# Kernel tuning notes

Hardware: AMD Instinct MI355X
Metric: run time of the kernel (lower is better)

The kernel has to match this reference:

```python
import jax, jax.numpy as jnp
import numpy as np

C = 256
H = W = 64
B = 8


def setup_inputs() -> dict:
    key = jax.random.key(0)
    ks = jax.random.split(key, 9)
    s = 1.0 / np.sqrt(C)
    x = jax.random.normal(ks[0], (B, C, H, W), dtype=jnp.float32)
    Wq = jax.random.normal(ks[1], (C, C), dtype=jnp.float32) * s
    bq = jnp.zeros((C,), dtype=jnp.float32)
    Wk = jax.random.normal(ks[2], (C, C), dtype=jnp.float32) * s
    bk = jnp.zeros((C,), dtype=jnp.float32)
    Wv = jax.random.normal(ks[3], (C, C), dtype=jnp.float32) * s
    bv = jnp.zeros((C,), dtype=jnp.float32)
    Wp = jax.random.normal(ks[4], (C, C), dtype=jnp.float32) * s
    bp = jnp.zeros((C,), dtype=jnp.float32)
    return {"x": x, "Wq": Wq, "bq": bq, "Wk": Wk, "bk": bk,
            "Wv": Wv, "bv": bv, "Wp": Wp, "bp": bp}


def reference(x, Wq, bq, Wk, bk, Wv, bv, Wp, bp):
    # NOTE: the original forward never calls self.norm, so GroupNorm is omitted.
    Bv_, Cv, Hv, Wv_ = x.shape
    N = Hv * Wv_
    xf = x.reshape(Bv_, Cv, N)  # [B, C, N]
    # 1x1 convs == per-pixel linear over channels
    q = jnp.einsum('oc,bcn->bno', Wq, xf) + bq            # [B, N, C]
    k = jnp.einsum('oc,bcn->bon', Wk, xf) + bk[:, None]   # [B, C, N]
    v = jnp.einsum('oc,bcn->bno', Wv, xf) + bv            # [B, N, C]
    scale = Cv ** (-0.5)
    attn = jnp.einsum('bnc,bcm->bnm', q, k) * scale       # [B, N, N]
    attn = jax.nn.softmax(attn, axis=-1)
    h = jnp.einsum('bnm,bmc->bnc', attn, v)               # [B, N, C]
    h = h.transpose(0, 2, 1).reshape(Bv_, Cv, Hv, Wv_)
    proj = jnp.einsum('oc,bcn->bon', Wp, xf) + bp[:, None]
    proj = proj.reshape(Bv_, Cv, Hv, Wv_)
    # residual uses proj(x) (applied to the INPUT), as in the original code
    return h + proj
```

## Files before the change

### kernel.cpp

```cpp
#include <hip/hip_runtime.h>

typedef __attribute__((ext_vector_type(8))) short short8;
typedef __attribute__((ext_vector_type(4))) short short4v;
typedef __attribute__((ext_vector_type(4))) float floatx4;
typedef unsigned int u32;

#define CC 256
#define NN 4096
#define NB 8

static __device__ __forceinline__ float b2f(ushort u) {
    union { unsigned int i; float f; } c;
    c.i = ((unsigned int)u) << 16;
    return c.f;
}

static __device__ __forceinline__ ushort f2bf(float f) {
    union { float f; unsigned int u; } c;
    c.f = f;
    unsigned int u = c.u;
    u += 0x7fffu + ((u >> 16) & 1u);
    return (ushort)(u >> 16);
}

static __device__ __forceinline__ short8 load8(const void* p, size_t idx, bool isbf) {
    if (isbf) {
        return *(const short8*)((const ushort*)p + idx);
    } else {
        const float* f = (const float*)p + idx;
        floatx4 a = *(const floatx4*)f;
        floatx4 b = *(const floatx4*)(f + 4);
        short8 r;
        #pragma unroll
        for (int j = 0; j < 4; j++) {
            ((ushort*)&r)[j]     = f2bf(a[j]);
            ((ushort*)&r)[j + 4] = f2bf(b[j]);
        }
        return r;
    }
}

static __device__ __forceinline__ float loadS(const void* p, size_t idx, bool isbf) {
    return isbf ? b2f(((const ushort*)p)[idx]) : ((const float*)p)[idx];
}

static __device__ __forceinline__ bool detect_bf16(const void* x) {
    const ushort* xu = (const ushort*)x;
    int cnt = 0;
    #pragma unroll
    for (int j = 0; j < 8; j++) {
        ushort u = xu[(size_t)j * 1048576];
        int e = (u >> 7) & 0xFF;
        cnt += ((e >= 100 && e <= 141) || (u & 0x7FFF) == 0) ? 1 : 0;
    }
    return cnt >= 7;
}

static __device__ __forceinline__ void gll16(const ushort* g, ushort* l) {
    __builtin_amdgcn_global_load_lds(
        (const __attribute__((address_space(1))) u32*)g,
        (__attribute__((address_space(3))) u32*)l, 16, 0, 0);
}

__global__ __launch_bounds__(256) void projkvpq(
    const void* __restrict__ x,
    const void* __restrict__ Wk, const void* __restrict__ bk,
    const void* __restrict__ Wv, const void* __restrict__ bv,
    const void* __restrict__ Wp, const void* __restrict__ bp,
    const void* __restrict__ Wq, const void* __restrict__ bq,
    ushort* __restrict__ k_ws, ushort* __restrict__ v_ws,
    ushort* __restrict__ q_ws, float* __restrict__ out, int b0)
{
    __shared__ __align__(16) ushort A_lds[4][64 * 40];
    __shared__ __align__(16) ushort Bt_lds[64 * 40];
    __shared__ __align__(16) ushort T_lds[64 * 72];

    const bool isbf = detect_bf16(x);
    const int tid  = threadIdx.x;
    const int wave = tid >> 6;
    const int lane = tid & 63;
    const int l16  = lane & 15;
    const int quad = lane >> 4;

    const int n0 = blockIdx.x * 64;
    const int o0 = blockIdx.y * 64;
    const int bl = blockIdx.z;
    const int b  = b0 + bl;

    floatx4 zero4 = {0.f, 0.f, 0.f, 0.f};
    floatx4 acc[4][4];
    #pragma unroll
    for (int w = 0; w < 4; w++)
        #pragma unroll
        for (int t = 0; t < 4; t++) acc[w][t] = zero4;

    const void* Ws[4] = {Wk, Wv, Wp, Wq};

    for (int k0 = 0; k0 < CC; k0 += 32) {
        __syncthreads();
        {
            int row = tid >> 2, c8 = (tid & 3) * 8;
            #pragma unroll
            for (int w = 0; w < 4; w++)
                *(short8*)&A_lds[w][row * 40 + c8] =
                    load8(Ws[w], (size_t)(o0 + row) * CC + k0 + c8, isbf);
        }
        {
            int c = tid >> 3, n8 = (tid & 7) * 8;
            short8 xv = load8(x, ((size_t)b * CC + k0 + c) * NN + n0 + n8, isbf);
            #pragma unroll
            for (int j = 0; j < 8; j++)
                Bt_lds[(n8 + j) * 40 + c] = ((ushort*)&xv)[j];
        }
        __syncthreads();

        short8 af[4];
        #pragma unroll
        for (int w = 0; w < 4; w++)
            af[w] = *(const short8*)&A_lds[w][(wave * 16 + l16) * 40 + quad * 8];
        #pragma unroll
        for (int t = 0; t < 4; t++) {
            short8 bf = *(const short8*)&Bt_lds[(t * 16 + l16) * 40 + quad * 8];
            #pragma unroll
            for (int w = 0; w < 4; w++)
                acc[w][t] = __builtin_amdgcn_mfma_f32_16x16x32_bf16(af[w], bf, acc[w][t], 0, 0, 0);
        }
    }

    float biasv[4][4];
    const void* Bs[4] = {bk, bv, bp, bq};
    #pragma unroll
    for (int w = 0; w < 4; w++)
        #pragma unroll
        for (int r = 0; r < 4; r++)
            biasv[w][r] = loadS(Bs[w], (size_t)(o0 + wave * 16 + quad * 4 + r), isbf);

    __syncthreads();
    #pragma unroll
    for (int t = 0; t < 4; t++)
        #pragma unroll
        for (int r = 0; r < 4; r++)
            T_lds[(t * 16 + l16) * 72 + wave * 16 + quad * 4 + r] =
                f2bf(acc[0][t][r] + biasv[0][r]);
    __syncthreads();
    for (int u = tid; u < 512; u += 256) {
        int n = u >> 3, o8 = (u & 7) * 8;
        *(short8*)&k_ws[((size_t)bl * NN + n0 + n) * CC + o0 + o8] =
            *(const short8*)&T_lds[n * 72 + o8];
    }

    __syncthreads();
    #pragma unroll
    for (int t = 0; t < 4; t++)
        #pragma unroll
        for (int r = 0; r < 4; r++)
            T_lds[(t * 16 + l16) * 72 + wave * 16 + quad * 4 + r] =
                f2bf((acc[3][t][r] + biasv[3][r]) * 0.0625f);
    __syncthreads();
    for (int u = tid; u < 512; u += 256) {
        int n = u >> 3, o8 = (u & 7) * 8;
        *(short8*)&q_ws[((size_t)bl * NN + n0 + n) * CC + o0 + o8] =
            *(const short8*)&T_lds[n * 72 + o8];
    }

    __syncthreads();
    #pragma unroll
    for (int t = 0; t < 4; t++)
        #pragma unroll
        for (int r = 0; r < 4; r++)
            T_lds[(wave * 16 + quad * 4 + r) * 72 + t * 16 + l16] =
                f2bf(acc[1][t][r] + biasv[1][r]);
    __syncthreads();
    for (int u = tid; u < 512; u += 256) {
        int o = u >> 3, n8 = (u & 7) * 8;
        *(short8*)&v_ws[((size_t)bl * CC + o0 + o) * NN + n0 + n8] =
            *(const short8*)&T_lds[o * 72 + n8];
    }

    #pragma unroll
    for (int t = 0; t < 4; t++)
        #pragma unroll
        for (int r = 0; r < 4; r++)
            out[((size_t)b * CC + o0 + wave * 16 + quad * 4 + r) * NN +
                n0 + t * 16 + l16] = acc[2][t][r] + biasv[2][r];
}

__global__ __launch_bounds__(512) void attn_mfma(
    const ushort* __restrict__ q_ws, const ushort* __restrict__ k_ws,
    const ushort* __restrict__ v_ws, float* __restrict__ out,
    float* __restrict__ po, float* __restrict__ ml, int b0, int nsplit)
{
    __shared__ __align__(16) ushort lds[33792];
    ushort* K_lds  = lds;
    ushort* Vt_lds = lds + 8192;
    ushort* P_lds  = lds + 16384;
    float*  Tf     = (float*)lds;

    const int tid  = threadIdx.x;
    const int wave = tid >> 6;
    const int lane = tid & 63;
    const int l16  = lane & 15;
    const int quad = lane >> 4;
    const int bl = blockIdx.y;
    const int b  = b0 + bl;
    const int n0 = blockIdx.x * 256;
    const int hs = blockIdx.z;

    floatx4 zero4 = {0.f, 0.f, 0.f, 0.f};

    const ushort* qp = q_ws + ((size_t)bl * NN + n0 + wave * 32 + l16) * CC;
    short8 qf[2][8];
    #pragma unroll
    for (int f = 0; f < 2; f++)
        #pragma unroll
        for (int s = 0; s < 8; s++)
            qf[f][s] = *(const short8*)&qp[(size_t)(f * 16) * CC + s * 32 + quad * 8];

    const ushort* kp = k_ws + (size_t)bl * NN * CC;
    const ushort* vp = v_ws + (size_t)bl * CC * NN;

    floatx4 Oacc[2][16];
    #pragma unroll
    for (int f = 0; f < 2; f++)
        #pragma unroll
        for (int t = 0; t < 16; t++) Oacc[f][t] = zero4;
    float mrow[2] = {-1e30f, -1e30f}, lrow[2] = {0.f, 0.f};

    const int NT  = (NN / 32) / nsplit;
    const int it0 = hs * NT;

    #pragma unroll 1
    for (int it = it0; it < it0 + NT; ++it) {
        const int m0 = it * 32;
        __syncthreads();

        #pragma unroll
        for (int i = 0; i < 2; i++) {
            int c = wave * 2 + i;
            {
                int row = c * 2 + (lane >> 5);
                int sw  = (lane & 31) ^ (row & 7);
                gll16(kp + (size_t)(m0 + row) * CC + sw * 8, K_lds + c * 512);
            }
            {
                int ch = c * 16 + (lane >> 2);
                gll16(vp + (size_t)ch * NN + m0 + (lane & 3) * 8, Vt_lds + c * 512);
            }
        }
        __syncthreads();

        floatx4 S[2][2];
        S[0][0] = zero4; S[0][1] = zero4; S[1][0] = zero4; S[1][1] = zero4;
        #pragma unroll
        for (int t = 0; t < 2; t++) {
            int row = t * 16 + l16;
            int rsw = row & 7;
            #pragma unroll
            for (int s = 0; s < 8; s++) {
                short8 kf = *(const short8*)&K_lds[row * 256 + ((s * 4 + quad) ^ rsw) * 8];
                S[0][t] = __builtin_amdgcn_mfma_f32_16x16x32_bf16(kf, qf[0][s], S[0][t], 0, 0, 0);
                S[1][t] = __builtin_amdgcn_mfma_f32_16x16x32_bf16(kf, qf[1][s], S[1][t], 0, 0, 0);
            }
        }

        float mx[2];
        #pragma unroll
        for (int f = 0; f < 2; f++) {
            float m = fmaxf(fmaxf(fmaxf(S[f][0][0], S[f][0][1]),
                                  fmaxf(S[f][0][2], S[f][0][3])),
                            fmaxf(fmaxf(S[f][1][0], S[f][1][1]),
                                  fmaxf(S[f][1][2], S[f][1][3])));
            m = fmaxf(m, __shfl_xor(m, 16, 64));
            m = fmaxf(m, __shfl_xor(m, 32, 64));
            mx[f] = m;
        }

        if (__any((mx[0] - mrow[0] > 8.0f) || (mx[1] - mrow[1] > 8.0f))) {
            float a[2][4];
            #pragma unroll
            for (int f = 0; f < 2; f++) {
                float mn = fmaxf(mrow[f], mx[f]);
                float al = __expf(mrow[f] - mn);
                mrow[f] = mn;
                lrow[f] *= al;
                #pragma unroll
                for (int r = 0; r < 4; r++) a[f][r] = __shfl(al, quad * 4 + r, 64);
            }
            #pragma unroll
            for (int f = 0; f < 2; f++)
                #pragma unroll
                for (int ct = 0; ct < 16; ct++)
                    #pragma unroll
                    for (int r = 0; r < 4; r++)
                        Oacc[f][ct][r] *= a[f][r];
        }

        #pragma unroll
        for (int f = 0; f < 2; f++) {
            short4v w0, w1;
            float rs = 0.f;
            #pragma unroll
            for (int r = 0; r < 4; r++) {
                float p0 = __expf(S[f][0][r] - mrow[f]);
                float p1 = __expf(S[f][1][r] - mrow[f]);
                rs += p0 + p1;
                ((ushort*)&w0)[r] = f2bf(p0);
                ((ushort*)&w1)[r] = f2bf(p1);
            }
            rs += __shfl_xor(rs, 16, 64);
            rs += __shfl_xor(rs, 32, 64);
            lrow[f] += rs;
            int base = wave * 1280 + (f * 16 + l16) * 40 + quad * 4;
            *(short4v*)&P_lds[base]      = w0;
            *(short4v*)&P_lds[base + 16] = w1;
        }

        asm volatile("s_waitcnt lgkmcnt(0)" ::: "memory");
        __builtin_amdgcn_sched_barrier(0);

        short8 pf0 = *(const short8*)&P_lds[wave * 1280 + l16 * 40 + quad * 8];
        short8 pf1 = *(const short8*)&P_lds[wave * 1280 + (16 + l16) * 40 + quad * 8];
        #pragma unroll
        for (int ct = 0; ct < 16; ct++) {
            int ch = ct * 16 + l16;
            short8 vf = *(const short8*)&Vt_lds[ch * 32 + quad * 8];
            Oacc[0][ct] = __builtin_amdgcn_mfma_f32_16x16x32_bf16(pf0, vf, Oacc[0][ct], 0, 0, 0);
            Oacc[1][ct] = __builtin_amdgcn_mfma_f32_16x16x32_bf16(pf1, vf, Oacc[1][ct], 0, 0, 0);
        }
    }

    if (nsplit == 1) {
        float linv[2][4];
        #pragma unroll
        for (int f = 0; f < 2; f++) {
            float li = 1.0f / lrow[f];
            #pragma unroll
            for (int r = 0; r < 4; r++) linv[f][r] = __shfl(li, quad * 4 + r, 64);
        }
        #pragma unroll
        for (int c0 = 0; c0 < 4; c0++) {
            __syncthreads();
            #pragma unroll
            for (int j = 0; j < 4; j++) {
                int ct = c0 * 4 + j;
                #pragma unroll
                for (int f = 0; f < 2; f++)
                    #pragma unroll
                    for (int r = 0; r < 4; r++)
                        Tf[(j * 16 + l16) * 264 + wave * 32 + f * 16 + quad * 4 + r] =
                            Oacc[f][ct][r] * linv[f][r];
            }
            __syncthreads();
            #pragma unroll
            for (int i = 0; i < 8; i++) {
                int u = tid + i * 512;
                int chl = u >> 6, col4 = (u & 63) * 4;
                size_t gi = ((size_t)b * CC + c0 * 64 + chl) * NN + n0 + col4;
                floatx4 pv = *(const floatx4*)&out[gi];
                floatx4 tv = *(const floatx4*)&Tf[chl * 264 + col4];
                pv[0] += tv[0]; pv[1] += tv[1]; pv[2] += tv[2]; pv[3] += tv[3];
                *(floatx4*)&out[gi] = pv;
            }
        }
    } else {
        const int pidx = (hs * NB + b) * (NN / 256) + blockIdx.x;
        float* pO = po + (size_t)pidx * (256 * 256);
        if (quad == 0) {
            #pragma unroll
            for (int f = 0; f < 2; f++) {
                int row = wave * 32 + f * 16 + l16;
                ml[(size_t)pidx * 512 + row]       = mrow[f];
                ml[(size_t)pidx * 512 + 256 + row] = lrow[f];
            }
        }
        #pragma unroll
        for (int c0 = 0; c0 < 4; c0++) {
            __syncthreads();
            #pragma unroll
            for (int j = 0; j < 4; j++) {
                int ct = c0 * 4 + j;
                #pragma unroll
                for (int f = 0; f < 2; f++)
                    #pragma unroll
                    for (int r = 0; r < 4; r++)
                        Tf[(j * 16 + l16) * 264 + wave * 32 + f * 16 + quad * 4 + r] =
                            Oacc[f][ct][r];
            }
            __syncthreads();
            #pragma unroll
            for (int i = 0; i < 8; i++) {
                int u = tid + i * 512;
                int chl = u >> 6, col4 = (u & 63) * 4;
                *(floatx4*)&pO[(size_t)(c0 * 64 + chl) * 256 + col4] =
                    *(const floatx4*)&Tf[chl * 264 + col4];
            }
        }
    }
}

__global__ __launch_bounds__(256) void attn_merge(
    const float* __restrict__ po, const float* __restrict__ ml,
    float* __restrict__ out, int b0)
{
    __shared__ float sm[4][256];
    const int ntile = blockIdx.x;
    const int b = b0 + blockIdx.y;
    const int NT2 = NN / 256;
    const int p0 = (0 * NB + b) * NT2 + ntile;
    const int p1 = (1 * NB + b) * NT2 + ntile;
    const float* O0 = po + (size_t)p0 * (256 * 256);
    const float* O1 = po + (size_t)p1 * (256 * 256);
    const int tid = threadIdx.x;
    sm[0][tid] = ml[(size_t)p0 * 512 + tid];
    sm[1][tid] = ml[(size_t)p0 * 512 + 256 + tid];
    sm[2][tid] = ml[(size_t)p1 * 512 + tid];
    sm[3][tid] = ml[(size_t)p1 * 512 + 256 + tid];
    __syncthreads();

    const int c = tid;
    float* op = out + ((size_t)b * CC + c) * NN + ntile * 256;
    const float* a = O0 + (size_t)c * 256;
    const float* d = O1 + (size_t)c * 256;
    #pragma unroll 4
    for (int r4 = 0; r4 < 256; r4 += 4) {
        floatx4 va = *(const floatx4*)&a[r4];
        floatx4 vd = *(const floatx4*)&d[r4];
        floatx4 vo = *(const floatx4*)&op[r4];
        #pragma unroll
        for (int j = 0; j < 4; j++) {
            int row = r4 + j;
            float m0 = sm[0][row], l0 = sm[1][row];
            float m1 = sm[2][row], l1 = sm[3][row];
            float M  = fmaxf(m0, m1);
            float w0 = __expf(m0 - M), w1 = __expf(m1 - M);
            float L  = l0 * w0 + l1 * w1;
            vo[j] += (va[j] * w0 + vd[j] * w1) / L;
        }
        *(floatx4*)&op[r4] = vo;
    }
}

extern "C" void kernel_launch(void* const* d_in, const int* in_sizes, int n_in,
                              void* d_out, int out_size, void* d_ws, size_t ws_size,
                              hipStream_t stream) {
    int xi = 0;
    for (int i = 0; i < n_in; i++)
        if (in_sizes[i] == NB * CC * NN) xi = i;

    const void *x, *Wq, *bq, *Wk, *bk, *Wv, *bv, *Wp, *bp;
    if (xi == 0) {
        x  = d_in[0];
        Wq = d_in[1]; bq = d_in[2];
        Wk = d_in[3]; bk = d_in[4];
        Wv = d_in[5]; bv = d_in[6];
        Wp = d_in[7]; bp = d_in[8];
    } else {
        int wi[4], bi[4], nw = 0, nb = 0;
        for (int i = 0; i < n_in; i++) {
            if (i == xi) continue;
            if (in_sizes[i] == CC * CC) { if (nw < 4) wi[nw++] = i; }
            else                        { if (nb < 4) bi[nb++] = i; }
        }
        x  = d_in[xi];
        Wk = d_in[wi[0]]; Wp = d_in[wi[1]]; Wq = d_in[wi[2]]; Wv = d_in[wi[3]];
        bk = d_in[bi[0]]; bp = d_in[bi[1]]; bq = d_in[bi[2]]; bv = d_in[bi[3]];
    }

    float*  out = (float*)d_out;
    ushort* ws  = (ushort*)d_ws;

    const size_t tsz_b = (size_t)NN * CC;
    int BC = 8;
    while (BC > 1 && (size_t)BC * tsz_b * 2 * 3 > ws_size) BC >>= 1;
    ushort* k_ws = ws;
    ushort* v_ws = ws + (size_t)BC * tsz_b;
    ushort* q_ws = ws + 2 * (size_t)BC * tsz_b;

    const size_t base_bytes = (size_t)3 * BC * tsz_b * 2;
    const size_t po_elems   = (size_t)2 * NB * (NN / 256) * 256 * 256;
    const size_t ml_elems   = (size_t)2 * NB * (NN / 256) * 512;
    const int nsplit = (BC == 8 &&
                        ws_size >= base_bytes + (po_elems + ml_elems) * 4) ? 2 : 1;
    float* po = (float*)(ws + 3 * (size_t)BC * tsz_b);
    float* ml = po + po_elems;

    for (int c0 = 0; c0 < NB; c0 += BC) {
        projkvpq<<<dim3(NN / 64, CC / 64, BC), dim3(256), 0, stream>>>(
            x, Wk, bk, Wv, bv, Wp, bp, Wq, bq, k_ws, v_ws, q_ws, out, c0);
        attn_mfma<<<dim3(NN / 256, BC, nsplit), dim3(512), 0, stream>>>(
            q_ws, k_ws, v_ws, out, po, ml, c0, nsplit);
        if (nsplit == 2)
            attn_merge<<<dim3(NN / 256, BC), dim3(256), 0, stream>>>(
                po, ml, out, c0);
    }
}
```

Baseline: 380.6 us.

## Double-buffer K/V tiles in attention loop to overlap loads with MFMA

Splits the K and V shared-memory tiles into two buffers and prefetches the next key block while computing on the current one. A partial vmcnt wait keeps only the current tile's loads outstanding, and raw barriers replace the two __syncthreads per iteration. This hides global-to-LDS latency behind the QK and PV MFMA work. In exchange, LDS use grows from about 66KB to 84KB, which may reduce blocks per CU, and correctness depends on the hand-counted vmcnt value.

```diff
diff --git a/kernel.cpp b/kernel.cpp
--- a/kernel.cpp
+++ b/kernel.cpp
@@ -190,10 +190,12 @@
     const ushort* __restrict__ v_ws, float* __restrict__ out,
     float* __restrict__ po, float* __restrict__ ml, int b0, int nsplit)
 {
-    __shared__ __align__(16) ushort lds[33792];
-    ushort* K_lds  = lds;
-    ushort* Vt_lds = lds + 8192;
-    ushort* P_lds  = lds + 16384;
+    __shared__ __align__(16) ushort lds[43008];
+    ushort* K0_lds = lds;
+    ushort* K1_lds = lds + 8192;
+    ushort* V0_lds = lds + 16384;
+    ushort* V1_lds = lds + 24576;
+    ushort* P_lds  = lds + 32768;
     float*  Tf     = (float*)lds;
 
     const int tid  = threadIdx.x;
@@ -228,26 +230,40 @@
 
     const int NT  = (NN / 32) / nsplit;
     const int it0 = hs * NT;
-
-    #pragma unroll 1
-    for (int it = it0; it < it0 + NT; ++it) {
-        const int m0 = it * 32;
-        __syncthreads();
-
+    const int itE = it0 + NT;
+
+    auto stage = [&](int it, ushort* kb, ushort* vb) {
+        int m0 = it * 32;
         #pragma unroll
         for (int i = 0; i < 2; i++) {
             int c = wave * 2 + i;
             {
                 int row = c * 2 + (lane >> 5);
                 int sw  = (lane & 31) ^ (row & 7);
-                gll16(kp + (size_t)(m0 + row) * CC + sw * 8, K_lds + c * 512);
+                gll16(kp + (size_t)(m0 + row) * CC + sw * 8, kb + c * 512);
             }
             {
                 int ch = c * 16 + (lane >> 2);
-                gll16(vp + (size_t)ch * NN + m0 + (lane & 3) * 8, Vt_lds + c * 512);
-            }
-        }
-        __syncthreads();
+                gll16(vp + (size_t)ch * NN + m0 + (lane & 3) * 8, vb + c * 512);
+            }
+        }
+    };
+
+    stage(it0, K0_lds, V0_lds);
+
+    #pragma unroll 1
+    for (int it = it0; it < itE; ++it) {
+        const int cb = (it - it0) & 1;
+        ushort* Kc = cb ? K1_lds : K0_lds;
+        ushort* Vc = cb ? V1_lds : V0_lds;
+
+        if (it + 1 < itE) {
+            stage(it + 1, cb ? K0_lds : K1_lds, cb ? V0_lds : V1_lds);
+            asm volatile("s_waitcnt vmcnt(4)" ::: "memory");
+        } else {
+            asm volatile("s_waitcnt vmcnt(0)" ::: "memory");
+        }
+        __builtin_amdgcn_s_barrier();
 
         floatx4 S[2][2];
         S[0][0] = zero4; S[0][1] = zero4; S[1][0] = zero4; S[1][1] = zero4;
@@ -257,7 +273,7 @@
             int rsw = row & 7;
             #pragma unroll
             for (int s = 0; s < 8; s++) {
-                short8 kf = *(const short8*)&K_lds[row * 256 + ((s * 4 + quad) ^ rsw) * 8];
+                short8 kf = *(const short8*)&Kc[row * 256 + ((s * 4 + quad) ^ rsw) * 8];
                 S[0][t] = __builtin_amdgcn_mfma_f32_16x16x32_bf16(kf, qf[0][s], S[0][t], 0, 0, 0);
                 S[1][t] = __builtin_amdgcn_mfma_f32_16x16x32_bf16(kf, qf[1][s], S[1][t], 0, 0, 0);
             }
@@ -323,10 +339,14 @@
         #pragma unroll
         for (int ct = 0; ct < 16; ct++) {
             int ch = ct * 16 + l16;
-            short8 vf = *(const short8*)&Vt_lds[ch * 32 + quad * 8];
+            short8 vf = *(const short8*)&Vc[ch * 32 + quad * 8];
             Oacc[0][ct] = __builtin_amdgcn_mfma_f32_16x16x32_bf16(pf0, vf, Oacc[0][ct], 0, 0, 0);
             Oacc[1][ct] = __builtin_amdgcn_mfma_f32_16x16x32_bf16(pf1, vf, Oacc[1][ct], 0, 0, 0);
         }
+
+        asm volatile("s_waitcnt lgkmcnt(0)" ::: "memory");
+        __builtin_amdgcn_sched_barrier(0);
+        __builtin_amdgcn_s_barrier();
     }
 
     if (nsplit == 1) {
```

Result: faster. 356.4 us (-6.4%).
